# Performance work log

Measured on AMD Instinct MI355X. Metric: run time of the kernel, lower is better.

## Reference

```python
import jax, jax.numpy as jnp
import numpy as np

B, C, H, W = 4, 256, 64, 64


def setup_inputs() -> dict:
    key = jax.random.key(0)
    k1, k2, k3, k4 = jax.random.split(key, 4)
    inp = jax.random.normal(k1, (B, C, H, W), dtype=jnp.float32)
    inter_mask = jnp.ones((B, 1, H, W), dtype=jnp.float32)
    flow_init = jax.random.normal(k2, (B, 2, H, W), dtype=jnp.float32)
    # nn.Linear(C, C): weight [out,in], bias [out]
    lim = 1.0 / np.sqrt(C)
    W_lin = jax.random.uniform(k3, (C, C), dtype=jnp.float32, minval=-lim, maxval=lim)
    b_lin = jax.random.uniform(k4, (C,), dtype=jnp.float32, minval=-lim, maxval=lim)
    return {"inp": inp, "inter_mask": inter_mask, "flow_init": flow_init,
            "W_lin": W_lin, "b_lin": b_lin}


def reference(inp, inter_mask, flow_init, W_lin, b_lin):
    batch, ch, ht, wd = inp.shape
    n = ht * wd
    # [B, N, C]
    x = inp.reshape(batch, ch, n).transpose(0, 2, 1)
    x = x @ W_lin.T + b_lin
    scale = ch ** (-0.5)
    # [B, N, N] full self-correlation
    scores = jnp.einsum('bnc,bmc->bnm', x * scale, x)
    attn = jax.nn.softmax(scores, axis=-1)
    # [B, N, 2]
    flow = flow_init.reshape(batch, 2, n).transpose(0, 2, 1)
    flow_add = attn @ flow
    # [B, 2, H, W]
    return flow_add.reshape(batch, ht, wd, 2).transpose(0, 3, 1, 2)
```

## Files before the change

kernel.cpp:

```cpp
#include <hip/hip_runtime.h>
#include <hip/hip_bf16.h>

#define NB 4
#define CCH 256
#define NN 4096
#define QT 128
#define KSPLIT 4
#define MRANGE (NN / KSPLIT)
#define MTILE 64
#define NTILES (MRANGE / MTILE)
#define VPAD 8

#define SQRTK 0.30028060f

typedef __attribute__((ext_vector_type(8))) short short8;
typedef __attribute__((ext_vector_type(16))) float f32x16;
typedef __attribute__((ext_vector_type(4))) int i32x4;

__device__ inline ushort f2bf(float f) {
    uint u = __float_as_uint(f);
    uint r = (u + 0x7fffu + ((u >> 16) & 1u)) >> 16;
    return (ushort)r;
}

__device__ inline float dev_exp2(float x) {
#if __has_builtin(__builtin_amdgcn_exp2f)
    return __builtin_amdgcn_exp2f(x);
#else
    return exp2f(x);
#endif
}

__device__ inline void gl_lds16(const void* g, void* l) {
    __builtin_amdgcn_global_load_lds(
        (const __attribute__((address_space(1))) unsigned int*)g,
        (__attribute__((address_space(3))) unsigned int*)l, 16, 0, 0);
}

__global__ __launch_bounds__(256) void transp_k(const float* __restrict__ inp,
                                                ushort* __restrict__ inpT,
                                                const float* __restrict__ W,
                                                ushort* __restrict__ Wb) {
    if (blockIdx.x >= 1024) {
        int i = (blockIdx.x - 1024) * 256 + threadIdx.x;
        float4 v = reinterpret_cast<const float4*>(W)[i];
        ushort4 r;
        r.x = f2bf(v.x); r.y = f2bf(v.y); r.z = f2bf(v.z); r.w = f2bf(v.w);
        reinterpret_cast<ushort4*>(Wb)[i] = r;
        return;
    }
    int wg = blockIdx.x;
    int nblk = wg & 63, cblk = (wg >> 6) & 3, b = wg >> 8;
    __shared__ float tile[64 * 67];
    int t = threadIdx.x;
    const float* src = inp + ((size_t)(b * CCH + cblk * 64)) * NN + nblk * 64;
#pragma unroll
    for (int p = 0; p < 4; p++) {
        int ci = p * 256 + t;
        int c = ci >> 4, n4 = ci & 15;
        float4 v = *reinterpret_cast<const float4*>(src + (size_t)c * NN + n4 * 4);
        float* d = &tile[c * 67 + n4 * 4];
        d[0] = v.x; d[1] = v.y; d[2] = v.z; d[3] = v.w;
    }
    __syncthreads();
    ushort* dst = inpT + ((size_t)(b * NN + nblk * 64)) * CCH + cblk * 64;
#pragma unroll
    for (int p = 0; p < 2; p++) {
        int u = p * 256 + t;
        int n = u >> 3, cc = u & 7;
        ushort tmp[8];
#pragma unroll
        for (int j = 0; j < 8; j++) tmp[j] = f2bf(tile[(cc * 8 + j) * 67 + n]);
        uint4 o;
        o.x = (uint)tmp[0] | ((uint)tmp[1] << 16);
        o.y = (uint)tmp[2] | ((uint)tmp[3] << 16);
        o.z = (uint)tmp[4] | ((uint)tmp[5] << 16);
        o.w = (uint)tmp[6] | ((uint)tmp[7] << 16);
        *reinterpret_cast<uint4*>(dst + (size_t)n * CCH + cc * 8) = o;
    }
}

__global__ __launch_bounds__(256) void linear_k(const ushort* __restrict__ inpT,
                                                const ushort* __restrict__ Wb,
                                                const float* __restrict__ bias,
                                                ushort* __restrict__ xs) {
    int wg = blockIdx.x;
    int b = wg >> 6, nt = wg & 63;
    int t = threadIdx.x, l = t & 63, w = t >> 6;
    int nbase = nt * 64 + (w & 1) * 32;
    int obase = (w >> 1) * 128;
    const ushort* arow = inpT + ((size_t)(b * NN + nbase + (l & 31))) * CCH + ((l >> 5) * 8);
    const ushort* wrow = Wb + ((size_t)(obase + (l & 31))) * CCH + ((l >> 5) * 8);
    f32x16 acc[4];
#pragma unroll
    for (int os = 0; os < 4; os++)
#pragma unroll
        for (int r = 0; r < 16; r++) acc[os][r] = 0.f;

#pragma unroll
    for (int ch = 0; ch < 16; ch++) {
        short8 a = *reinterpret_cast<const short8*>(arow + ch * 16);
#pragma unroll
        for (int os = 0; os < 4; os++) {
            short8 bb = *reinterpret_cast<const short8*>(wrow + (size_t)os * 32 * CCH + ch * 16);
            acc[os] = __builtin_amdgcn_mfma_f32_32x32x16_bf16(a, bb, acc[os], 0, 0, 0);
        }
    }
#pragma unroll
    for (int os = 0; os < 4; os++) {
        int oc = obase + os * 32 + (l & 31);
        float bv = bias[oc];
#pragma unroll
        for (int r = 0; r < 16; r++) {
            int row = (r & 3) + 8 * (r >> 2) + 4 * (l >> 5);
            float v = (acc[os][r] + bv) * SQRTK;
            xs[((size_t)(b * NN + nt * 64 + (w & 1) * 32 + row)) * CCH + oc] = f2bf(v);
        }
    }
}

__global__ __launch_bounds__(256) void attn_k(const ushort* __restrict__ xs,
                                              const float* __restrict__ flow,
                                              float* __restrict__ part) {
    int wg = blockIdx.x;
    int b = wg >> 7;
    int qt = (wg >> 2) & 31;
    int ks = wg & 3;
    int t = threadIdx.x, l = t & 63, w = t >> 6;
    const ushort* xb = xs + (size_t)b * NN * CCH;
    int qbase = qt * QT + w * 32;
    int mstart = ks * MRANGE;

    __shared__ ushort kt[2][MTILE * 256];
    __shared__ ushort vlds[4][MRANGE + VPAD];

    {
        int m0 = t * 4;
        float4 fx4 = *reinterpret_cast<const float4*>(flow + (size_t)b * 2 * NN + mstart + m0);
        float4 fy4 = *reinterpret_cast<const float4*>(flow + (size_t)b * 2 * NN + NN + mstart + m0);
        float fxv[4] = {fx4.x, fx4.y, fx4.z, fx4.w};
        float fyv[4] = {fy4.x, fy4.y, fy4.z, fy4.w};
#pragma unroll
        for (int i = 0; i < 4; i++) {
            int m = m0 + i, ml = m & 15;
            int pos = (m & ~15) | (ml & 3) | ((ml & 4) << 1) | ((ml & 8) >> 1);
            vlds[0][pos] = f2bf(fxv[i]);
            vlds[1][pos] = f2bf(fyv[i]);
            vlds[2][pos] = 0x3F80;
            vlds[3][pos] = 0;
        }
    }

    short8 qf[16];
    const ushort* qrow = xb + ((size_t)(qbase + (l & 31))) * CCH + (l >> 5) * 8;
#pragma unroll
    for (int ch = 0; ch < 16; ch++)
        qf[ch] = *reinterpret_cast<const short8*>(qrow + ch * 16);

    f32x16 pv;
#pragma unroll
    for (int r = 0; r < 16; r++) pv[r] = 0.f;

    auto stage = [&](int buf, int tile) {
        int mb = mstart + tile * MTILE;
        const char* src = (const char*)(xb + (size_t)mb * CCH);
#pragma unroll
        for (int p = 0; p < 8; p++) {
            int chunk = w * 8 + p;
            int lin = chunk * 1024 + l * 16;
            int row = lin >> 9;
            int cb = lin & 511;
            int gsw = cb ^ ((row & 15) << 4);
            gl_lds16(src + (size_t)row * 512 + gsw, &kt[buf][chunk * 512]);
        }
    };

    int c_sel = (l & 31) < 3 ? (l & 31) : 3;
    stage(0, 0);
    __syncthreads();
    int cur = 0;
    for (int tile = 0; tile < NTILES; tile++) {
        if (tile + 1 < NTILES) stage(cur ^ 1, tile + 1);
#pragma unroll
        for (int ms = 0; ms < 2; ms++) {
            f32x16 S;
#pragma unroll
            for (int r = 0; r < 16; r++) S[r] = 0.f;
            const char* base = (const char*)&kt[cur][(ms * 32 + (l & 31)) * 256];
            int swz = (l & 15) << 4;
#pragma unroll
            for (int ch = 0; ch < 16; ch++) {
                int cbyte = (ch * 32 + ((l >> 5) * 16)) ^ swz;
                short8 kf = *reinterpret_cast<const short8*>(base + cbyte);
                S = __builtin_amdgcn_mfma_f32_32x32x16_bf16(kf, qf[ch], S, 0, 0, 0);
            }
#pragma unroll
            for (int r = 0; r < 16; r++) S[r] = dev_exp2(S[r]);
            uint wd[8];
#pragma unroll
            for (int p = 0; p < 8; p++) {
                float lo = S[2 * p], hi = S[2 * p + 1];
                asm("v_cvt_pk_bf16_f32 %0, %1, %2" : "=v"(wd[p]) : "v"(lo), "v"(hi));
            }
            i32x4 lo4 = {(int)wd[0], (int)wd[1], (int)wd[2], (int)wd[3]};
            i32x4 hi4 = {(int)wd[4], (int)wd[5], (int)wd[6], (int)wd[7]};
            short8 pa0 = __builtin_bit_cast(short8, lo4);
            short8 pa1 = __builtin_bit_cast(short8, hi4);
            int mloc = tile * MTILE + ms * 32;
            const ushort* vb = &vlds[c_sel][mloc + (l >> 5) * 8];
            short8 v0 = *reinterpret_cast<const short8*>(vb);
            short8 v1 = *reinterpret_cast<const short8*>(vb + 16);
            pv = __builtin_amdgcn_mfma_f32_32x32x16_bf16(pa0, v0, pv, 0, 0, 0);
            pv = __builtin_amdgcn_mfma_f32_32x32x16_bf16(pa1, v1, pv, 0, 0, 0);
        }
        __syncthreads();
        cur ^= 1;
    }

    int c = l & 31;
    if (c < 3) {
        float* pb = part + ((size_t)(b * KSPLIT + ks)) * 3 * NN;
        int off = ((c + 1) % 3) * NN;
#pragma unroll
        for (int r = 0; r < 16; r++) {
            int row = (r & 3) + 8 * (r >> 2) + 4 * (l >> 5);
            pb[off + qbase + row] = pv[r];
        }
    }
}

__global__ void finalize_k(const float* __restrict__ part, float* __restrict__ out) {
    int i = blockIdx.x * 256 + threadIdx.x;
    int b = i >> 12, n = i & 4095;
    float s = 0.f, x = 0.f, y = 0.f;
#pragma unroll
    for (int ks = 0; ks < KSPLIT; ks++) {
        const float* p = part + ((size_t)(b * KSPLIT + ks)) * 3 * NN;
        s += p[n];
        x += p[NN + n];
        y += p[2 * NN + n];
    }
    out[(size_t)b * 2 * NN + n] = x / s;
    out[(size_t)b * 2 * NN + NN + n] = y / s;
}

extern "C" void kernel_launch(void* const* d_in, const int* in_sizes, int n_in,
                              void* d_out, int out_size, void* d_ws, size_t ws_size,
                              hipStream_t stream) {
    const float* inp  = (const float*)d_in[0];
    const float* flow = (const float*)d_in[2];
    const float* W    = (const float*)d_in[3];
    const float* bias = (const float*)d_in[4];
    float* out = (float*)d_out;

    char* ws = (char*)d_ws;
    ushort* xs   = (ushort*)(ws);
    ushort* inpT = (ushort*)(ws + 8388608);
    ushort* Wb   = (ushort*)(ws + 16777216);
    float*  part = (float*)(ws + 8388608);

    transp_k<<<1088, 256, 0, stream>>>(inp, inpT, W, Wb);
    linear_k<<<256, 256, 0, stream>>>(inpT, Wb, bias, xs);
    attn_k<<<512, 256, 0, stream>>>(xs, flow, part);
    finalize_k<<<64, 256, 0, stream>>>(part, out);
}
```

Baseline: 65.79 us.

## Fuse transpose into linear kernel and double query rows per wave in attention

Folds the input transpose/bf16 conversion into the linear kernel via LDS staging, removing the inpT round trip through global memory and one launch. The attention kernel now has each wave process 64 query rows (two accumulator sets), so each K tile loaded into LDS is reused twice as much. KSPLIT is raised to 8 to keep the grid at 512 blocks, with launch_bounds(256,2) set. The change raises register pressure from the doubled Q fragments and accumulators, and the fused linear kernel serializes the transpose ahead of its MFMA work.

```diff
diff --git a/kernel.cpp b/kernel.cpp
--- a/kernel.cpp
+++ b/kernel.cpp
@@ -4,8 +4,8 @@
 #define NB 4
 #define CCH 256
 #define NN 4096
-#define QT 128
-#define KSPLIT 4
+#define QT 256
+#define KSPLIT 8
 #define MRANGE (NN / KSPLIT)
 #define MTILE 64
 #define NTILES (MRANGE / MTILE)
@@ -37,59 +37,54 @@
         (__attribute__((address_space(3))) unsigned int*)l, 16, 0, 0);
 }
 
-__global__ __launch_bounds__(256) void transp_k(const float* __restrict__ inp,
-                                                ushort* __restrict__ inpT,
-                                                const float* __restrict__ W,
-                                                ushort* __restrict__ Wb) {
-    if (blockIdx.x >= 1024) {
-        int i = (blockIdx.x - 1024) * 256 + threadIdx.x;
-        float4 v = reinterpret_cast<const float4*>(W)[i];
-        ushort4 r;
-        r.x = f2bf(v.x); r.y = f2bf(v.y); r.z = f2bf(v.z); r.w = f2bf(v.w);
-        reinterpret_cast<ushort4*>(Wb)[i] = r;
-        return;
-    }
-    int wg = blockIdx.x;
-    int nblk = wg & 63, cblk = (wg >> 6) & 3, b = wg >> 8;
-    __shared__ float tile[64 * 67];
-    int t = threadIdx.x;
-    const float* src = inp + ((size_t)(b * CCH + cblk * 64)) * NN + nblk * 64;
-#pragma unroll
-    for (int p = 0; p < 4; p++) {
-        int ci = p * 256 + t;
-        int c = ci >> 4, n4 = ci & 15;
-        float4 v = *reinterpret_cast<const float4*>(src + (size_t)c * NN + n4 * 4);
-        float* d = &tile[c * 67 + n4 * 4];
-        d[0] = v.x; d[1] = v.y; d[2] = v.z; d[3] = v.w;
-    }
-    __syncthreads();
-    ushort* dst = inpT + ((size_t)(b * NN + nblk * 64)) * CCH + cblk * 64;
-#pragma unroll
-    for (int p = 0; p < 2; p++) {
-        int u = p * 256 + t;
-        int n = u >> 3, cc = u & 7;
-        ushort tmp[8];
-#pragma unroll
-        for (int j = 0; j < 8; j++) tmp[j] = f2bf(tile[(cc * 8 + j) * 67 + n]);
-        uint4 o;
-        o.x = (uint)tmp[0] | ((uint)tmp[1] << 16);
-        o.y = (uint)tmp[2] | ((uint)tmp[3] << 16);
-        o.z = (uint)tmp[4] | ((uint)tmp[5] << 16);
-        o.w = (uint)tmp[6] | ((uint)tmp[7] << 16);
-        *reinterpret_cast<uint4*>(dst + (size_t)n * CCH + cc * 8) = o;
-    }
-}
-
-__global__ __launch_bounds__(256) void linear_k(const ushort* __restrict__ inpT,
-                                                const ushort* __restrict__ Wb,
-                                                const float* __restrict__ bias,
-                                                ushort* __restrict__ xs) {
+__global__ void wconv_k(const float* __restrict__ W, ushort* __restrict__ Wb) {
+    int i = blockIdx.x * 256 + threadIdx.x;
+    float4 v = reinterpret_cast<const float4*>(W)[i];
+    ushort4 r;
+    r.x = f2bf(v.x); r.y = f2bf(v.y); r.z = f2bf(v.z); r.w = f2bf(v.w);
+    reinterpret_cast<ushort4*>(Wb)[i] = r;
+}
+
+__global__ __launch_bounds__(256) void fusedlin_k(const float* __restrict__ inp,
+                                                  const ushort* __restrict__ Wb,
+                                                  const float* __restrict__ bias,
+                                                  ushort* __restrict__ xs) {
     int wg = blockIdx.x;
     int b = wg >> 6, nt = wg & 63;
     int t = threadIdx.x, l = t & 63, w = t >> 6;
-    int nbase = nt * 64 + (w & 1) * 32;
+    __shared__ float ftile[64 * 67];
+    __shared__ ushort xtile[64][260];
+
+    for (int cblk = 0; cblk < 4; cblk++) {
+        const float* src = inp + ((size_t)(b * CCH + cblk * 64)) * NN + nt * 64;
+#pragma unroll
+        for (int p = 0; p < 4; p++) {
+            int ci = p * 256 + t;
+            int c = ci >> 4, n4 = ci & 15;
+            float4 v = *reinterpret_cast<const float4*>(src + (size_t)c * NN + n4 * 4);
+            float* d = &ftile[c * 67 + n4 * 4];
+            d[0] = v.x; d[1] = v.y; d[2] = v.z; d[3] = v.w;
+        }
+        __syncthreads();
+#pragma unroll
+        for (int p = 0; p < 2; p++) {
+            int u = p * 256 + t;
+            int n = u >> 3, cc = u & 7;
+            ushort tmp[8];
+#pragma unroll
+            for (int j = 0; j < 8; j++) tmp[j] = f2bf(ftile[(cc * 8 + j) * 67 + n]);
+            uint4 o;
+            o.x = (uint)tmp[0] | ((uint)tmp[1] << 16);
+            o.y = (uint)tmp[2] | ((uint)tmp[3] << 16);
+            o.z = (uint)tmp[4] | ((uint)tmp[5] << 16);
+            o.w = (uint)tmp[6] | ((uint)tmp[7] << 16);
+            *reinterpret_cast<uint4*>(&xtile[n][cblk * 64 + cc * 8]) = o;
+        }
+        __syncthreads();
+    }
+
+    int nb = (w & 1) * 32;
     int obase = (w >> 1) * 128;
-    const ushort* arow = inpT + ((size_t)(b * NN + nbase + (l & 31))) * CCH + ((l >> 5) * 8);
     const ushort* wrow = Wb + ((size_t)(obase + (l & 31))) * CCH + ((l >> 5) * 8);
     f32x16 acc[4];
 #pragma unroll
@@ -97,9 +92,10 @@
 #pragma unroll
         for (int r = 0; r < 16; r++) acc[os][r] = 0.f;
 
+    const char* arow = (const char*)&xtile[nb + (l & 31)][0] + (l >> 5) * 16;
 #pragma unroll
     for (int ch = 0; ch < 16; ch++) {
-        short8 a = *reinterpret_cast<const short8*>(arow + ch * 16);
+        short8 a = *reinterpret_cast<const short8*>(arow + ch * 32);
 #pragma unroll
         for (int os = 0; os < 4; os++) {
             short8 bb = *reinterpret_cast<const short8*>(wrow + (size_t)os * 32 * CCH + ch * 16);
@@ -114,34 +110,34 @@
         for (int r = 0; r < 16; r++) {
             int row = (r & 3) + 8 * (r >> 2) + 4 * (l >> 5);
             float v = (acc[os][r] + bv) * SQRTK;
-            xs[((size_t)(b * NN + nt * 64 + (w & 1) * 32 + row)) * CCH + oc] = f2bf(v);
-        }
-    }
-}
-
-__global__ __launch_bounds__(256) void attn_k(const ushort* __restrict__ xs,
-                                              const float* __restrict__ flow,
-                                              float* __restrict__ part) {
+            xs[((size_t)(b * NN + nt * 64 + nb + row)) * CCH + oc] = f2bf(v);
+        }
+    }
+}
+
+__global__ __launch_bounds__(256, 2) void attn_k(const ushort* __restrict__ xs,
+                                                 const float* __restrict__ flow,
+                                                 float* __restrict__ part) {
     int wg = blockIdx.x;
     int b = wg >> 7;
-    int qt = (wg >> 2) & 31;
-    int ks = wg & 3;
+    int qt = (wg >> 3) & 15;
+    int ks = wg & 7;
     int t = threadIdx.x, l = t & 63, w = t >> 6;
     const ushort* xb = xs + (size_t)b * NN * CCH;
-    int qbase = qt * QT + w * 32;
+    int qbase = qt * QT + w * 64;
     int mstart = ks * MRANGE;
 
     __shared__ ushort kt[2][MTILE * 256];
     __shared__ ushort vlds[4][MRANGE + VPAD];
 
     {
-        int m0 = t * 4;
-        float4 fx4 = *reinterpret_cast<const float4*>(flow + (size_t)b * 2 * NN + mstart + m0);
-        float4 fy4 = *reinterpret_cast<const float4*>(flow + (size_t)b * 2 * NN + NN + mstart + m0);
-        float fxv[4] = {fx4.x, fx4.y, fx4.z, fx4.w};
-        float fyv[4] = {fy4.x, fy4.y, fy4.z, fy4.w};
-#pragma unroll
-        for (int i = 0; i < 4; i++) {
+        int m0 = t * 2;
+        float2 fx2 = *reinterpret_cast<const float2*>(flow + (size_t)b * 2 * NN + mstart + m0);
+        float2 fy2 = *reinterpret_cast<const float2*>(flow + (size_t)b * 2 * NN + NN + mstart + m0);
+        float fxv[2] = {fx2.x, fx2.y};
+        float fyv[2] = {fy2.x, fy2.y};
+#pragma unroll
+        for (int i = 0; i < 2; i++) {
             int m = m0 + i, ml = m & 15;
             int pos = (m & ~15) | (ml & 3) | ((ml & 4) << 1) | ((ml & 8) >> 1);
             vlds[0][pos] = f2bf(fxv[i]);
@@ -151,15 +147,18 @@
         }
     }
 
-    short8 qf[16];
-    const ushort* qrow = xb + ((size_t)(qbase + (l & 31))) * CCH + (l >> 5) * 8;
-#pragma unroll
-    for (int ch = 0; ch < 16; ch++)
-        qf[ch] = *reinterpret_cast<const short8*>(qrow + ch * 16);
-
-    f32x16 pv;
-#pragma unroll
-    for (int r = 0; r < 16; r++) pv[r] = 0.f;
+    short8 qf0[16], qf1[16];
+    const ushort* qrow0 = xb + ((size_t)(qbase + (l & 31))) * CCH + (l >> 5) * 8;
+    const ushort* qrow1 = qrow0 + (size_t)32 * CCH;
+#pragma unroll
+    for (int ch = 0; ch < 16; ch++) {
+        qf0[ch] = *reinterpret_cast<const short8*>(qrow0 + ch * 16);
+        qf1[ch] = *reinterpret_cast<const short8*>(qrow1 + ch * 16);
+    }
+
+    f32x16 pv0, pv1;
+#pragma unroll
+    for (int r = 0; r < 16; r++) { pv0[r] = 0.f; pv1[r] = 0.f; }
 
     auto stage = [&](int buf, int tile) {
         int mb = mstart + tile * MTILE;
@@ -183,35 +182,42 @@
         if (tile + 1 < NTILES) stage(cur ^ 1, tile + 1);
 #pragma unroll
         for (int ms = 0; ms < 2; ms++) {
-            f32x16 S;
-#pragma unroll
-            for (int r = 0; r < 16; r++) S[r] = 0.f;
+            f32x16 S0, S1;
+#pragma unroll
+            for (int r = 0; r < 16; r++) { S0[r] = 0.f; S1[r] = 0.f; }
             const char* base = (const char*)&kt[cur][(ms * 32 + (l & 31)) * 256];
             int swz = (l & 15) << 4;
 #pragma unroll
             for (int ch = 0; ch < 16; ch++) {
                 int cbyte = (ch * 32 + ((l >> 5) * 16)) ^ swz;
                 short8 kf = *reinterpret_cast<const short8*>(base + cbyte);
-                S = __builtin_amdgcn_mfma_f32_32x32x16_bf16(kf, qf[ch], S, 0, 0, 0);
+                S0 = __builtin_amdgcn_mfma_f32_32x32x16_bf16(kf, qf0[ch], S0, 0, 0, 0);
+                S1 = __builtin_amdgcn_mfma_f32_32x32x16_bf16(kf, qf1[ch], S1, 0, 0, 0);
             }
 #pragma unroll
-            for (int r = 0; r < 16; r++) S[r] = dev_exp2(S[r]);
-            uint wd[8];
+            for (int r = 0; r < 16; r++) { S0[r] = dev_exp2(S0[r]); S1[r] = dev_exp2(S1[r]); }
+            uint wa[8], wb2[8];
 #pragma unroll
             for (int p = 0; p < 8; p++) {
-                float lo = S[2 * p], hi = S[2 * p + 1];
-                asm("v_cvt_pk_bf16_f32 %0, %1, %2" : "=v"(wd[p]) : "v"(lo), "v"(hi));
+                asm("v_cvt_pk_bf16_f32 %0, %1, %2" : "=v"(wa[p]) : "v"(S0[2 * p]), "v"(S0[2 * p + 1]));
+                asm("v_cvt_pk_bf16_f32 %0, %1, %2" : "=v"(wb2[p]) : "v"(S1[2 * p]), "v"(S1[2 * p + 1]));
             }
-            i32x4 lo4 = {(int)wd[0], (int)wd[1], (int)wd[2], (int)wd[3]};
-            i32x4 hi4 = {(int)wd[4], (int)wd[5], (int)wd[6], (int)wd[7]};
-            short8 pa0 = __builtin_bit_cast(short8, lo4);
-            short8 pa1 = __builtin_bit_cast(short8, hi4);
+            i32x4 a0 = {(int)wa[0], (int)wa[1], (int)wa[2], (int)wa[3]};
+            i32x4 a1 = {(int)wa[4], (int)wa[5], (int)wa[6], (int)wa[7]};
+            i32x4 b0 = {(int)wb2[0], (int)wb2[1], (int)wb2[2], (int)wb2[3]};
+            i32x4 b1 = {(int)wb2[4], (int)wb2[5], (int)wb2[6], (int)wb2[7]};
+            short8 pa00 = __builtin_bit_cast(short8, a0);
+            short8 pa01 = __builtin_bit_cast(short8, a1);
+            short8 pa10 = __builtin_bit_cast(short8, b0);
+            short8 pa11 = __builtin_bit_cast(short8, b1);
             int mloc = tile * MTILE + ms * 32;
             const ushort* vb = &vlds[c_sel][mloc + (l >> 5) * 8];
             short8 v0 = *reinterpret_cast<const short8*>(vb);
             short8 v1 = *reinterpret_cast<const short8*>(vb + 16);
-            pv = __builtin_amdgcn_mfma_f32_32x32x16_bf16(pa0, v0, pv, 0, 0, 0);
-            pv = __builtin_amdgcn_mfma_f32_32x32x16_bf16(pa1, v1, pv, 0, 0, 0);
+            pv0 = __builtin_amdgcn_mfma_f32_32x32x16_bf16(pa00, v0, pv0, 0, 0, 0);
+            pv0 = __builtin_amdgcn_mfma_f32_32x32x16_bf16(pa01, v1, pv0, 0, 0, 0);
+            pv1 = __builtin_amdgcn_mfma_f32_32x32x16_bf16(pa10, v0, pv1, 0, 0, 0);
+            pv1 = __builtin_amdgcn_mfma_f32_32x32x16_bf16(pa11, v1, pv1, 0, 0, 0);
         }
         __syncthreads();
         cur ^= 1;
@@ -224,7 +230,8 @@
 #pragma unroll
         for (int r = 0; r < 16; r++) {
             int row = (r & 3) + 8 * (r >> 2) + 4 * (l >> 5);
-            pb[off + qbase + row] = pv[r];
+            pb[off + qbase + row] = pv0[r];
+            pb[off + qbase + 32 + row] = pv1[r];
         }
     }
 }
@@ -255,12 +262,11 @@
 
     char* ws = (char*)d_ws;
     ushort* xs   = (ushort*)(ws);
-    ushort* inpT = (ushort*)(ws + 8388608);
+    float*  part = (float*)(ws + 8388608);
     ushort* Wb   = (ushort*)(ws + 16777216);
-    float*  part = (float*)(ws + 8388608);
-
-    transp_k<<<1088, 256, 0, stream>>>(inp, inpT, W, Wb);
-    linear_k<<<256, 256, 0, stream>>>(inpT, Wb, bias, xs);
+
+    wconv_k<<<64, 256, 0, stream>>>(W, Wb);
+    fusedlin_k<<<256, 256, 0, stream>>>(inp, Wb, bias, xs);
     attn_k<<<512, 256, 0, stream>>>(xs, flow, part);
     finalize_k<<<64, 256, 0, stream>>>(part, out);
 }
```

Measured after the change: 67.01 us. No clear change (+1.8%).

## Fuse transpose into linear kernel and restructure attention to direct global K loads

Applied to the files above, without the earlier changes.

Folds the input transpose and bf16 conversion into the linear kernel, staging through shared memory, so the intermediate transposed buffer no longer goes through global memory. The attention kernel now gives each wave its own key range of 512 (KSPLIT 8) for a 32-query tile and reads K fragments straight from global memory, dropping the LDS double buffer and the per-tile barriers. Grid sizes double and launch bounds request higher occupancy. The trade-off is that K is no longer shared through LDS across waves, so reuse now depends on the caches, and the partial-sum count doubles.

```diff
diff --git a/kernel.cpp b/kernel.cpp
--- a/kernel.cpp
+++ b/kernel.cpp
@@ -4,12 +4,10 @@
 #define NB 4
 #define CCH 256
 #define NN 4096
-#define QT 128
-#define KSPLIT 4
+#define KSPLIT 8
 #define MRANGE (NN / KSPLIT)
-#define MTILE 64
+#define MTILE 32
 #define NTILES (MRANGE / MTILE)
-#define VPAD 8
 
 #define SQRTK 0.30028060f
 
@@ -31,117 +29,106 @@
 #endif
 }
 
-__device__ inline void gl_lds16(const void* g, void* l) {
-    __builtin_amdgcn_global_load_lds(
-        (const __attribute__((address_space(1))) unsigned int*)g,
-        (__attribute__((address_space(3))) unsigned int*)l, 16, 0, 0);
-}
-
-__global__ __launch_bounds__(256) void transp_k(const float* __restrict__ inp,
-                                                ushort* __restrict__ inpT,
-                                                const float* __restrict__ W,
-                                                ushort* __restrict__ Wb) {
-    if (blockIdx.x >= 1024) {
-        int i = (blockIdx.x - 1024) * 256 + threadIdx.x;
-        float4 v = reinterpret_cast<const float4*>(W)[i];
-        ushort4 r;
-        r.x = f2bf(v.x); r.y = f2bf(v.y); r.z = f2bf(v.z); r.w = f2bf(v.w);
-        reinterpret_cast<ushort4*>(Wb)[i] = r;
-        return;
-    }
+__global__ void wconv_k(const float* __restrict__ W, ushort* __restrict__ Wb) {
+    int i = blockIdx.x * 256 + threadIdx.x;
+    float4 v = reinterpret_cast<const float4*>(W)[i];
+    ushort4 r;
+    r.x = f2bf(v.x); r.y = f2bf(v.y); r.z = f2bf(v.z); r.w = f2bf(v.w);
+    reinterpret_cast<ushort4*>(Wb)[i] = r;
+}
+
+__global__ __launch_bounds__(256) void fusedlin_k(const float* __restrict__ inp,
+                                                  const ushort* __restrict__ Wb,
+                                                  const float* __restrict__ bias,
+                                                  ushort* __restrict__ xs) {
     int wg = blockIdx.x;
-    int nblk = wg & 63, cblk = (wg >> 6) & 3, b = wg >> 8;
-    __shared__ float tile[64 * 67];
-    int t = threadIdx.x;
-    const float* src = inp + ((size_t)(b * CCH + cblk * 64)) * NN + nblk * 64;
-#pragma unroll
-    for (int p = 0; p < 4; p++) {
-        int ci = p * 256 + t;
-        int c = ci >> 4, n4 = ci & 15;
-        float4 v = *reinterpret_cast<const float4*>(src + (size_t)c * NN + n4 * 4);
-        float* d = &tile[c * 67 + n4 * 4];
-        d[0] = v.x; d[1] = v.y; d[2] = v.z; d[3] = v.w;
-    }
-    __syncthreads();
-    ushort* dst = inpT + ((size_t)(b * NN + nblk * 64)) * CCH + cblk * 64;
-#pragma unroll
-    for (int p = 0; p < 2; p++) {
-        int u = p * 256 + t;
-        int n = u >> 3, cc = u & 7;
-        ushort tmp[8];
-#pragma unroll
-        for (int j = 0; j < 8; j++) tmp[j] = f2bf(tile[(cc * 8 + j) * 67 + n]);
-        uint4 o;
-        o.x = (uint)tmp[0] | ((uint)tmp[1] << 16);
-        o.y = (uint)tmp[2] | ((uint)tmp[3] << 16);
-        o.z = (uint)tmp[4] | ((uint)tmp[5] << 16);
-        o.w = (uint)tmp[6] | ((uint)tmp[7] << 16);
-        *reinterpret_cast<uint4*>(dst + (size_t)n * CCH + cc * 8) = o;
-    }
-}
-
-__global__ __launch_bounds__(256) void linear_k(const ushort* __restrict__ inpT,
-                                                const ushort* __restrict__ Wb,
-                                                const float* __restrict__ bias,
-                                                ushort* __restrict__ xs) {
-    int wg = blockIdx.x;
-    int b = wg >> 6, nt = wg & 63;
+    int b = wg >> 7, nt = wg & 127;
     int t = threadIdx.x, l = t & 63, w = t >> 6;
-    int nbase = nt * 64 + (w & 1) * 32;
-    int obase = (w >> 1) * 128;
-    const ushort* arow = inpT + ((size_t)(b * NN + nbase + (l & 31))) * CCH + ((l >> 5) * 8);
+    __shared__ float ftile[64 * 33];
+    __shared__ ushort xtile[32][260];
+
+    for (int cblk = 0; cblk < 4; cblk++) {
+        const float* src = inp + ((size_t)(b * CCH + cblk * 64)) * NN + nt * 32;
+#pragma unroll
+        for (int p = 0; p < 2; p++) {
+            int ci = p * 256 + t;
+            int c = ci >> 3, n4 = ci & 7;
+            float4 v = *reinterpret_cast<const float4*>(src + (size_t)c * NN + n4 * 4);
+            float* d = &ftile[c * 33 + n4 * 4];
+            d[0] = v.x; d[1] = v.y; d[2] = v.z; d[3] = v.w;
+        }
+        __syncthreads();
+        {
+            int n = t >> 3, cc = t & 7;
+            ushort tmp[8];
+#pragma unroll
+            for (int j = 0; j < 8; j++) tmp[j] = f2bf(ftile[(cc * 8 + j) * 33 + n]);
+            uint4 o;
+            o.x = (uint)tmp[0] | ((uint)tmp[1] << 16);
+            o.y = (uint)tmp[2] | ((uint)tmp[3] << 16);
+            o.z = (uint)tmp[4] | ((uint)tmp[5] << 16);
+            o.w = (uint)tmp[6] | ((uint)tmp[7] << 16);
+            *reinterpret_cast<uint4*>(&xtile[n][cblk * 64 + cc * 8]) = o;
+        }
+        __syncthreads();
+    }
+
+    int obase = w * 64;
     const ushort* wrow = Wb + ((size_t)(obase + (l & 31))) * CCH + ((l >> 5) * 8);
-    f32x16 acc[4];
-#pragma unroll
-    for (int os = 0; os < 4; os++)
+    f32x16 acc[2];
+#pragma unroll
+    for (int os = 0; os < 2; os++)
 #pragma unroll
         for (int r = 0; r < 16; r++) acc[os][r] = 0.f;
 
+    const char* arow = (const char*)&xtile[l & 31][0] + (l >> 5) * 16;
 #pragma unroll
     for (int ch = 0; ch < 16; ch++) {
-        short8 a = *reinterpret_cast<const short8*>(arow + ch * 16);
-#pragma unroll
-        for (int os = 0; os < 4; os++) {
+        short8 a = *reinterpret_cast<const short8*>(arow + ch * 32);
+#pragma unroll
+        for (int os = 0; os < 2; os++) {
             short8 bb = *reinterpret_cast<const short8*>(wrow + (size_t)os * 32 * CCH + ch * 16);
             acc[os] = __builtin_amdgcn_mfma_f32_32x32x16_bf16(a, bb, acc[os], 0, 0, 0);
         }
     }
 #pragma unroll
-    for (int os = 0; os < 4; os++) {
+    for (int os = 0; os < 2; os++) {
         int oc = obase + os * 32 + (l & 31);
         float bv = bias[oc];
 #pragma unroll
         for (int r = 0; r < 16; r++) {
             int row = (r & 3) + 8 * (r >> 2) + 4 * (l >> 5);
             float v = (acc[os][r] + bv) * SQRTK;
-            xs[((size_t)(b * NN + nt * 64 + (w & 1) * 32 + row)) * CCH + oc] = f2bf(v);
-        }
-    }
-}
-
-__global__ __launch_bounds__(256) void attn_k(const ushort* __restrict__ xs,
-                                              const float* __restrict__ flow,
-                                              float* __restrict__ part) {
+            xs[((size_t)(b * NN + nt * 32 + row)) * CCH + oc] = f2bf(v);
+        }
+    }
+}
+
+__global__ __launch_bounds__(256, 4) void attn_k(const ushort* __restrict__ xs,
+                                                 const float* __restrict__ flow,
+                                                 float* __restrict__ part) {
     int wg = blockIdx.x;
-    int b = wg >> 7;
-    int qt = (wg >> 2) & 31;
-    int ks = wg & 3;
+    int b = wg >> 8;
+    int qt = (wg >> 1) & 127;
+    int kp = wg & 1;
     int t = threadIdx.x, l = t & 63, w = t >> 6;
     const ushort* xb = xs + (size_t)b * NN * CCH;
-    int qbase = qt * QT + w * 32;
+    int qbase = qt * 32;
+    int ks = kp * 4 + w;
     int mstart = ks * MRANGE;
 
-    __shared__ ushort kt[2][MTILE * 256];
-    __shared__ ushort vlds[4][MRANGE + VPAD];
-
+    __shared__ alignas(16) ushort vlds[4][2048 + 8];
     {
-        int m0 = t * 4;
-        float4 fx4 = *reinterpret_cast<const float4*>(flow + (size_t)b * 2 * NN + mstart + m0);
-        float4 fy4 = *reinterpret_cast<const float4*>(flow + (size_t)b * 2 * NN + NN + mstart + m0);
-        float fxv[4] = {fx4.x, fx4.y, fx4.z, fx4.w};
-        float fyv[4] = {fy4.x, fy4.y, fy4.z, fy4.w};
-#pragma unroll
-        for (int i = 0; i < 4; i++) {
+        int m0 = t * 8;
+        int gm = kp * 2048 + m0;
+        float4 fx4a = *reinterpret_cast<const float4*>(flow + (size_t)b * 2 * NN + gm);
+        float4 fx4b = *reinterpret_cast<const float4*>(flow + (size_t)b * 2 * NN + gm + 4);
+        float4 fy4a = *reinterpret_cast<const float4*>(flow + (size_t)b * 2 * NN + NN + gm);
+        float4 fy4b = *reinterpret_cast<const float4*>(flow + (size_t)b * 2 * NN + NN + gm + 4);
+        float fxv[8] = {fx4a.x, fx4a.y, fx4a.z, fx4a.w, fx4b.x, fx4b.y, fx4b.z, fx4b.w};
+        float fyv[8] = {fy4a.x, fy4a.y, fy4a.z, fy4a.w, fy4b.x, fy4b.y, fy4b.z, fy4b.w};
+#pragma unroll
+        for (int i = 0; i < 8; i++) {
             int m = m0 + i, ml = m & 15;
             int pos = (m & ~15) | (ml & 3) | ((ml & 4) << 1) | ((ml & 8) >> 1);
             vlds[0][pos] = f2bf(fxv[i]);
@@ -157,64 +144,43 @@
     for (int ch = 0; ch < 16; ch++)
         qf[ch] = *reinterpret_cast<const short8*>(qrow + ch * 16);
 
+    __syncthreads();
+
     f32x16 pv;
 #pragma unroll
     for (int r = 0; r < 16; r++) pv[r] = 0.f;
 
-    auto stage = [&](int buf, int tile) {
-        int mb = mstart + tile * MTILE;
-        const char* src = (const char*)(xb + (size_t)mb * CCH);
+    int c_sel = (l & 31) < 3 ? (l & 31) : 3;
+    const ushort* kbase = xb + ((size_t)(mstart + (l & 31))) * CCH + (l >> 5) * 8;
+    int vbase_off = kp ? -2048 : 0;
+
+    for (int tile = 0; tile < NTILES; tile++) {
+        f32x16 S;
+#pragma unroll
+        for (int r = 0; r < 16; r++) S[r] = 0.f;
+        const ushort* kt = kbase + (size_t)(tile * MTILE) * CCH;
+#pragma unroll
+        for (int ch = 0; ch < 16; ch++) {
+            short8 kf = *reinterpret_cast<const short8*>(kt + ch * 16);
+            S = __builtin_amdgcn_mfma_f32_32x32x16_bf16(kf, qf[ch], S, 0, 0, 0);
+        }
+#pragma unroll
+        for (int r = 0; r < 16; r++) S[r] = dev_exp2(S[r]);
+        uint wd[8];
 #pragma unroll
         for (int p = 0; p < 8; p++) {
-            int chunk = w * 8 + p;
-            int lin = chunk * 1024 + l * 16;
-            int row = lin >> 9;
-            int cb = lin & 511;
-            int gsw = cb ^ ((row & 15) << 4);
-            gl_lds16(src + (size_t)row * 512 + gsw, &kt[buf][chunk * 512]);
-        }
-    };
-
-    int c_sel = (l & 31) < 3 ? (l & 31) : 3;
-    stage(0, 0);
-    __syncthreads();
-    int cur = 0;
-    for (int tile = 0; tile < NTILES; tile++) {
-        if (tile + 1 < NTILES) stage(cur ^ 1, tile + 1);
-#pragma unroll
-        for (int ms = 0; ms < 2; ms++) {
-            f32x16 S;
-#pragma unroll
-            for (int r = 0; r < 16; r++) S[r] = 0.f;
-            const char* base = (const char*)&kt[cur][(ms * 32 + (l & 31)) * 256];
-            int swz = (l & 15) << 4;
-#pragma unroll
-            for (int ch = 0; ch < 16; ch++) {
-                int cbyte = (ch * 32 + ((l >> 5) * 16)) ^ swz;
-                short8 kf = *reinterpret_cast<const short8*>(base + cbyte);
-                S = __builtin_amdgcn_mfma_f32_32x32x16_bf16(kf, qf[ch], S, 0, 0, 0);
-            }
-#pragma unroll
-            for (int r = 0; r < 16; r++) S[r] = dev_exp2(S[r]);
-            uint wd[8];
-#pragma unroll
-            for (int p = 0; p < 8; p++) {
-                float lo = S[2 * p], hi = S[2 * p + 1];
-                asm("v_cvt_pk_bf16_f32 %0, %1, %2" : "=v"(wd[p]) : "v"(lo), "v"(hi));
-            }
-            i32x4 lo4 = {(int)wd[0], (int)wd[1], (int)wd[2], (int)wd[3]};
-            i32x4 hi4 = {(int)wd[4], (int)wd[5], (int)wd[6], (int)wd[7]};
-            short8 pa0 = __builtin_bit_cast(short8, lo4);
-            short8 pa1 = __builtin_bit_cast(short8, hi4);
-            int mloc = tile * MTILE + ms * 32;
-            const ushort* vb = &vlds[c_sel][mloc + (l >> 5) * 8];
-            short8 v0 = *reinterpret_cast<const short8*>(vb);
-            short8 v1 = *reinterpret_cast<const short8*>(vb + 16);
-            pv = __builtin_amdgcn_mfma_f32_32x32x16_bf16(pa0, v0, pv, 0, 0, 0);
-            pv = __builtin_amdgcn_mfma_f32_32x32x16_bf16(pa1, v1, pv, 0, 0, 0);
-        }
-        __syncthreads();
-        cur ^= 1;
+            asm("v_cvt_pk_bf16_f32 %0, %1, %2" : "=v"(wd[p]) : "v"(S[2 * p]), "v"(S[2 * p + 1]));
+        }
+        i32x4 lo4 = {(int)wd[0], (int)wd[1], (int)wd[2], (int)wd[3]};
+        i32x4 hi4 = {(int)wd[4], (int)wd[5], (int)wd[6], (int)wd[7]};
+        short8 pa0 = __builtin_bit_cast(short8, lo4);
+        short8 pa1 = __builtin_bit_cast(short8, hi4);
+        int mloc = mstart + tile * MTILE + vbase_off;
+        const ushort* vb = &vlds[c_sel][mloc + (l >> 5) * 8];
+        short8 v0 = *reinterpret_cast<const short8*>(vb);
+        short8 v1 = *reinterpret_cast<const short8*>(vb + 16);
+        pv = __builtin_amdgcn_mfma_f32_32x32x16_bf16(pa0, v0, pv, 0, 0, 0);
+        pv = __builtin_amdgcn_mfma_f32_32x32x16_bf16(pa1, v1, pv, 0, 0, 0);
     }
 
     int c = l & 31;
@@ -255,12 +221,11 @@
 
     char* ws = (char*)d_ws;
     ushort* xs   = (ushort*)(ws);
-    ushort* inpT = (ushort*)(ws + 8388608);
+    float*  part = (float*)(ws + 8388608);
     ushort* Wb   = (ushort*)(ws + 16777216);
-    float*  part = (float*)(ws + 8388608);
-
-    transp_k<<<1088, 256, 0, stream>>>(inp, inpT, W, Wb);
-    linear_k<<<256, 256, 0, stream>>>(inpT, Wb, bias, xs);
-    attn_k<<<512, 256, 0, stream>>>(xs, flow, part);
+
+    wconv_k<<<64, 256, 0, stream>>>(W, Wb);
+    fusedlin_k<<<512, 256, 0, stream>>>(inp, Wb, bias, xs);
+    attn_k<<<1024, 256, 0, stream>>>(xs, flow, part);
     finalize_k<<<64, 256, 0, stream>>>(part, out);
 }
```

Result: slower. 150.2 us (+128.2%).

## Software-pipeline QK of the next tile against exp and PV of the current

Applied to the files above, without the earlier changes.

Restructures the attention loop so the QK MFMAs for tile t+1 run while the exp, bf16 pack and PV MFMAs of tile t are processed. The global-to-LDS staging for tile t+2 is issued in the same iteration. Both 32-row halves of a tile are computed together, and PV is split into two independent accumulators that are summed at the end, which breaks the MFMA dependency chain. A launch-bounds hint targets two workgroups per CU. The cost is more live registers (two extra S tiles and an extra accumulator), which could cause spills or lower occupancy.

```diff
diff --git a/kernel.cpp b/kernel.cpp
--- a/kernel.cpp
+++ b/kernel.cpp
@@ -119,9 +119,9 @@
     }
 }
 
-__global__ __launch_bounds__(256) void attn_k(const ushort* __restrict__ xs,
-                                              const float* __restrict__ flow,
-                                              float* __restrict__ part) {
+__global__ __launch_bounds__(256, 2) void attn_k(const ushort* __restrict__ xs,
+                                                 const float* __restrict__ flow,
+                                                 float* __restrict__ part) {
     int wg = blockIdx.x;
     int b = wg >> 7;
     int qt = (wg >> 2) & 31;
@@ -157,9 +157,9 @@
     for (int ch = 0; ch < 16; ch++)
         qf[ch] = *reinterpret_cast<const short8*>(qrow + ch * 16);
 
-    f32x16 pv;
-#pragma unroll
-    for (int r = 0; r < 16; r++) pv[r] = 0.f;
+    f32x16 pvA, pvB;
+#pragma unroll
+    for (int r = 0; r < 16; r++) { pvA[r] = 0.f; pvB[r] = 0.f; }
 
     auto stage = [&](int buf, int tile) {
         int mb = mstart + tile * MTILE;
@@ -175,46 +175,65 @@
         }
     };
 
+    auto qk = [&](int buf, f32x16& S0, f32x16& S1) {
+#pragma unroll
+        for (int r = 0; r < 16; r++) { S0[r] = 0.f; S1[r] = 0.f; }
+        const char* base0 = (const char*)&kt[buf][(l & 31) * 256];
+        const char* base1 = base0 + 32 * 512;
+        int swz = (l & 15) << 4;
+#pragma unroll
+        for (int ch = 0; ch < 16; ch++) {
+            int cbyte = (ch * 32 + ((l >> 5) * 16)) ^ swz;
+            short8 kf0 = *reinterpret_cast<const short8*>(base0 + cbyte);
+            short8 kf1 = *reinterpret_cast<const short8*>(base1 + cbyte);
+            S0 = __builtin_amdgcn_mfma_f32_32x32x16_bf16(kf0, qf[ch], S0, 0, 0, 0);
+            S1 = __builtin_amdgcn_mfma_f32_32x32x16_bf16(kf1, qf[ch], S1, 0, 0, 0);
+        }
+    };
+
     int c_sel = (l & 31) < 3 ? (l & 31) : 3;
+
     stage(0, 0);
     __syncthreads();
-    int cur = 0;
+    f32x16 Sp0, Sp1;
+    qk(0, Sp0, Sp1);
+    stage(1, 1);
+
+#pragma unroll 2
     for (int tile = 0; tile < NTILES; tile++) {
-        if (tile + 1 < NTILES) stage(cur ^ 1, tile + 1);
-#pragma unroll
-        for (int ms = 0; ms < 2; ms++) {
-            f32x16 S;
-#pragma unroll
-            for (int r = 0; r < 16; r++) S[r] = 0.f;
-            const char* base = (const char*)&kt[cur][(ms * 32 + (l & 31)) * 256];
-            int swz = (l & 15) << 4;
-#pragma unroll
-            for (int ch = 0; ch < 16; ch++) {
-                int cbyte = (ch * 32 + ((l >> 5) * 16)) ^ swz;
-                short8 kf = *reinterpret_cast<const short8*>(base + cbyte);
-                S = __builtin_amdgcn_mfma_f32_32x32x16_bf16(kf, qf[ch], S, 0, 0, 0);
-            }
-#pragma unroll
-            for (int r = 0; r < 16; r++) S[r] = dev_exp2(S[r]);
-            uint wd[8];
-#pragma unroll
-            for (int p = 0; p < 8; p++) {
-                float lo = S[2 * p], hi = S[2 * p + 1];
-                asm("v_cvt_pk_bf16_f32 %0, %1, %2" : "=v"(wd[p]) : "v"(lo), "v"(hi));
-            }
-            i32x4 lo4 = {(int)wd[0], (int)wd[1], (int)wd[2], (int)wd[3]};
-            i32x4 hi4 = {(int)wd[4], (int)wd[5], (int)wd[6], (int)wd[7]};
-            short8 pa0 = __builtin_bit_cast(short8, lo4);
-            short8 pa1 = __builtin_bit_cast(short8, hi4);
-            int mloc = tile * MTILE + ms * 32;
-            const ushort* vb = &vlds[c_sel][mloc + (l >> 5) * 8];
-            short8 v0 = *reinterpret_cast<const short8*>(vb);
-            short8 v1 = *reinterpret_cast<const short8*>(vb + 16);
-            pv = __builtin_amdgcn_mfma_f32_32x32x16_bf16(pa0, v0, pv, 0, 0, 0);
-            pv = __builtin_amdgcn_mfma_f32_32x32x16_bf16(pa1, v1, pv, 0, 0, 0);
-        }
         __syncthreads();
-        cur ^= 1;
+        f32x16 Sn0, Sn1;
+        if (tile + 1 < NTILES) qk((tile + 1) & 1, Sn0, Sn1);
+        if (tile + 2 < NTILES) stage(tile & 1, tile + 2);
+
+#pragma unroll
+        for (int r = 0; r < 16; r++) { Sp0[r] = dev_exp2(Sp0[r]); Sp1[r] = dev_exp2(Sp1[r]); }
+        uint wa[8], wb2[8];
+#pragma unroll
+        for (int p = 0; p < 8; p++) {
+            asm("v_cvt_pk_bf16_f32 %0, %1, %2" : "=v"(wa[p]) : "v"(Sp0[2 * p]), "v"(Sp0[2 * p + 1]));
+            asm("v_cvt_pk_bf16_f32 %0, %1, %2" : "=v"(wb2[p]) : "v"(Sp1[2 * p]), "v"(Sp1[2 * p + 1]));
+        }
+        i32x4 a0 = {(int)wa[0], (int)wa[1], (int)wa[2], (int)wa[3]};
+        i32x4 a1 = {(int)wa[4], (int)wa[5], (int)wa[6], (int)wa[7]};
+        i32x4 b0 = {(int)wb2[0], (int)wb2[1], (int)wb2[2], (int)wb2[3]};
+        i32x4 b1 = {(int)wb2[4], (int)wb2[5], (int)wb2[6], (int)wb2[7]};
+        short8 pa00 = __builtin_bit_cast(short8, a0);
+        short8 pa01 = __builtin_bit_cast(short8, a1);
+        short8 pa10 = __builtin_bit_cast(short8, b0);
+        short8 pa11 = __builtin_bit_cast(short8, b1);
+        const ushort* vb0 = &vlds[c_sel][tile * MTILE + (l >> 5) * 8];
+        const ushort* vb1 = vb0 + 32;
+        short8 v00 = *reinterpret_cast<const short8*>(vb0);
+        short8 v01 = *reinterpret_cast<const short8*>(vb0 + 16);
+        short8 v10 = *reinterpret_cast<const short8*>(vb1);
+        short8 v11 = *reinterpret_cast<const short8*>(vb1 + 16);
+        pvA = __builtin_amdgcn_mfma_f32_32x32x16_bf16(pa00, v00, pvA, 0, 0, 0);
+        pvB = __builtin_amdgcn_mfma_f32_32x32x16_bf16(pa10, v10, pvB, 0, 0, 0);
+        pvA = __builtin_amdgcn_mfma_f32_32x32x16_bf16(pa01, v01, pvA, 0, 0, 0);
+        pvB = __builtin_amdgcn_mfma_f32_32x32x16_bf16(pa11, v11, pvB, 0, 0, 0);
+
+        Sp0 = Sn0; Sp1 = Sn1;
     }
 
     int c = l & 31;
@@ -224,7 +243,7 @@
 #pragma unroll
         for (int r = 0; r < 16; r++) {
             int row = (r & 3) + 8 * (r >> 2) + 4 * (l >> 5);
-            pb[off + qbase + row] = pv[r];
+            pb[off + qbase + row] = pvA[r] + pvB[r];
         }
     }
 }
```

Result: faster. 63.32 us, median of 2 (-3.8%).
